# Optimization experiments

Measured on AMD Instinct MI355X. Metric: run time of the kernel, lower is better.

Reference implementation:

```python
import jax, jax.numpy as jnp
import numpy as np

N_FFT = 1024
HOP = 256
CACHE = N_FFT - 1  # causal left padding
EPS = 1e-12
BATCH = 16
SAMPLES = HOP * 2048


def _make_weight():
    # DFT basis modulated by a periodic Hann window (torch.hann_window default).
    n = np.arange(N_FFT, dtype=np.float32)
    k = np.arange(N_FFT // 2 + 1, dtype=np.float32)[:, None]
    ang = (-2.0 * np.pi / N_FFT) * k * n[None, :]
    win = 0.5 * (1.0 - np.cos(2.0 * np.pi * n / N_FFT))
    w = np.concatenate([np.cos(ang), np.sin(ang)], axis=0) * win  # [2*(N//2+1), N_FFT]
    return jnp.asarray(w, dtype=jnp.float32)[:, None, :]  # [O, I=1, K]


def setup_inputs() -> dict:
    key = jax.random.key(0)
    x = jax.random.normal(key, (BATCH, SAMPLES), dtype=jnp.float32)
    return {"x": x, "weight": _make_weight()}


def reference(x, weight):
    if x.ndim == 2:
        x = x[:, None, :]  # [B, 1, T]
    # causal constant (zero) padding on the left
    x = jnp.pad(x, ((0, 0), (0, 0), (CACHE, 0)))
    # strided conv against the fixed DFT basis: [B, 2*(N//2+1), L]
    y = jax.lax.conv_general_dilated(
        x, weight, window_strides=(HOP,), padding='VALID',
        dimension_numbers=('NCH', 'OIH', 'NCH'))
    B, C, T = y.shape
    y = y.reshape(B, 2, C // 2, T)  # real/imag split
    mag = jnp.sqrt(jnp.clip(jnp.sum(y * y, axis=1), EPS, None))  # [B, N//2+1, L]
    return mag
```

## Files before the change

kernel.cpp:

```cpp
#include <hip/hip_runtime.h>
#include <stdint.h>

#define SAMPLES   524288
#define BATCH     16
#define T_FRAMES  2048
#define HOPSZ     256
#define NCH       513
#define KF        512
#define MF        1152

#define SB_OFF    1183744
#define DB_OFF_1P (SB_OFF + 33554432)
#define WS_1P     (DB_OFF_1P + 33554432)
#define DB_OFF_2P 17960960

typedef __bf16          bf16x8 __attribute__((ext_vector_type(8)));
typedef float           f32x4  __attribute__((ext_vector_type(4)));
typedef unsigned short  u16x8  __attribute__((ext_vector_type(8)));

__device__ __forceinline__ unsigned short f2bf(float f) {
    union { float f; unsigned u; } v; v.f = f;
    unsigned r = v.u + 0x7fffu + ((v.u >> 16) & 1u);
    return (unsigned short)(r >> 16);
}

__global__ void prep(const float* __restrict__ x, const float* __restrict__ wsrc,
                     unsigned short* __restrict__ Wf,
                     unsigned short* __restrict__ Sb,
                     unsigned short* __restrict__ Db,
                     int batch0, int wblocks) {
    int bid = blockIdx.x;
    const int tid = threadIdx.x;
    if (bid < wblocks) {
        int gid = bid * 256 + tid;
        int m   = gid >> 6;
        int n0  = (gid & 63) << 3;
        int g = m >> 5, h = (m >> 4) & 1, r = m & 15;
        int bin = g * 16 + r;
        bool valid = h ? (bin >= 1 && bin <= 511) : (bin <= 512);
        const float* ws = wsrc + (long long)(h ? NCH + bin : bin) * 1024;
        union { u16x8 v; unsigned short e[8]; } o;
        #pragma unroll
        for (int e = 0; e < 8; ++e) {
            int n = n0 + e;
            float v = 0.f;
            if (valid) v = (n < 511) ? ws[n + 1] : 0.5f * ws[512];
            o.e[e] = f2bf(v);
        }
        *(u16x8*)(Wf + (long long)m * KF + n0) = o.v;
        return;
    }
    bid -= wblocks;
    const int fr = tid >> 6;
    const int n0 = (tid & 63) << 3;
    const long long f = (long long)bid * 4 + fr;
    const int bat = batch0 + (int)(f >> 11);
    const int t   = (int)(f & 2047);
    const float* xb = x + (long long)bat * SAMPLES;
    float fwd[8], rev[8];
    if (t >= 4) {
        const f32x4* pf = (const f32x4*)(xb + (t * 256 + n0 - 1024));
        f32x4 A = pf[0], B = pf[1], C = pf[2];
        fwd[0]=A[2]; fwd[1]=A[3]; fwd[2]=B[0]; fwd[3]=B[1];
        fwd[4]=B[2]; fwd[5]=B[3]; fwd[6]=C[0]; fwd[7]=C[1];
        const f32x4* pr = (const f32x4*)(xb + (t * 256 - n0 - 8));
        f32x4 D = pr[0], E = pr[1], F = pr[2];
        rev[0]=F[0]; rev[1]=E[3]; rev[2]=E[2]; rev[3]=E[1];
        rev[4]=E[0]; rev[5]=D[3]; rev[6]=D[2]; rev[7]=D[1];
    } else {
        #pragma unroll
        for (int e = 0; e < 8; ++e) {
            int n  = n0 + e;
            int pf = t * 256 + n + 1 - 1023;
            int pr = t * 256 - n;
            fwd[e] = (pf >= 0) ? xb[pf] : 0.f;
            rev[e] = (pr >= 0) ? xb[pr] : 0.f;
        }
    }
    union { u16x8 v; unsigned short e[8]; } so, dof;
    #pragma unroll
    for (int e = 0; e < 8; ++e) {
        so.e[e]  = f2bf(fwd[e] + rev[e]);
        dof.e[e] = f2bf(fwd[e] - rev[e]);
    }
    *(u16x8*)(Sb + f * KF + n0) = so.v;
    *(u16x8*)(Db + f * KF + n0) = dof.v;
}

__device__ __forceinline__ void gll16(const unsigned short* g, unsigned short* s) {
    __builtin_amdgcn_global_load_lds(
        (const __attribute__((address_space(1))) void*)g,
        (__attribute__((address_space(3))) void*)s,
        16, 0, 0);
}

__global__ __launch_bounds__(256, 3)
void stft_gemm(const unsigned short* __restrict__ Sb,
               const unsigned short* __restrict__ Db,
               const unsigned short* __restrict__ Wf,
               float* __restrict__ out, int batch0, int ftpx) {
    __shared__ unsigned short Ws[128 * 64];
    __shared__ unsigned short Ss[128 * 64];
    __shared__ unsigned short Ds[128 * 64];

    const int id  = blockIdx.x;
    const int xcd = id & 7;
    const int u   = id >> 3;
    const int ftl = u / 9;
    const int nt  = u - ftl * 9;
    const int ft  = xcd * ftpx + ftl;
    const int t0  = (ft & 15) * 128;
    const long long fl0 = (long long)ft * 128;

    const int tid = threadIdx.x;
    const int l   = tid & 63;
    const int w   = tid >> 6;
    const int ln  = l & 15;
    const int qd  = l >> 4;

    const int srow   = l >> 3;
    const int schunk = l & 7;

    const unsigned short* asrc[4];
    const unsigned short* ssrc[4];
    const unsigned short* dsrc[4];
    unsigned short* adst[4];
    unsigned short* sdst[4];
    unsigned short* ddst[4];
    #pragma unroll
    for (int c = 0; c < 4; ++c) {
        int r = w * 32 + c * 8 + srow;
        int gchunk = schunk ^ (r & 7);
        asrc[c] = Wf + (long long)(nt * 128 + r) * KF + gchunk * 8;
        ssrc[c] = Sb + (fl0 + r) * KF + gchunk * 8;
        dsrc[c] = Db + (fl0 + r) * KF + gchunk * 8;
        adst[c] = Ws + (w * 32 + c * 8) * 64;
        sdst[c] = Ss + (w * 32 + c * 8) * 64;
        ddst[c] = Ds + (w * 32 + c * 8) * 64;
    }

    const int wave_m = w & 1;
    const int wave_n = w >> 1;

    f32x4 acc[4][4];
    #pragma unroll
    for (int i = 0; i < 4; ++i)
        #pragma unroll
        for (int j = 0; j < 4; ++j)
            acc[i][j] = (f32x4){0.f, 0.f, 0.f, 0.f};

    int a_off[4][2], b_off[4][2];
    #pragma unroll
    for (int i = 0; i < 4; ++i)
        #pragma unroll
        for (int k2 = 0; k2 < 2; ++k2) {
            int ck = ((k2 * 4 + qd) ^ (ln & 7)) * 8;
            a_off[i][k2] = (wave_m * 64 + i * 16 + ln) * 64 + ck;
            b_off[i][k2] = (wave_n * 64 + i * 16 + ln) * 64 + ck;
        }

    for (int kk = 0; kk < KF; kk += 64) {
        #pragma unroll
        for (int c = 0; c < 4; ++c) gll16(asrc[c] + kk, adst[c]);
        #pragma unroll
        for (int c = 0; c < 4; ++c) gll16(ssrc[c] + kk, sdst[c]);
        #pragma unroll
        for (int c = 0; c < 4; ++c) gll16(dsrc[c] + kk, ddst[c]);
        __syncthreads();

        #pragma unroll
        for (int k2 = 0; k2 < 2; ++k2) {
            bf16x8 av[4], bs[4], bd[4];
            #pragma unroll
            for (int i = 0; i < 4; ++i) av[i] = *(const bf16x8*)&Ws[a_off[i][k2]];
            #pragma unroll
            for (int j = 0; j < 4; ++j) bs[j] = *(const bf16x8*)&Ss[b_off[j][k2]];
            #pragma unroll
            for (int j = 0; j < 4; ++j) bd[j] = *(const bf16x8*)&Ds[b_off[j][k2]];
            #pragma unroll
            for (int j = 0; j < 4; ++j) {
                acc[0][j] = __builtin_amdgcn_mfma_f32_16x16x32_bf16(av[0], bs[j], acc[0][j], 0, 0, 0);
                acc[1][j] = __builtin_amdgcn_mfma_f32_16x16x32_bf16(av[1], bd[j], acc[1][j], 0, 0, 0);
                acc[2][j] = __builtin_amdgcn_mfma_f32_16x16x32_bf16(av[2], bs[j], acc[2][j], 0, 0, 0);
                acc[3][j] = __builtin_amdgcn_mfma_f32_16x16x32_bf16(av[3], bd[j], acc[3][j], 0, 0, 0);
            }
        }
        __syncthreads();
    }

    const int b = batch0 + (ft >> 4);
    float* outb = out + (long long)b * (NCH * T_FRAMES);
    #pragma unroll
    for (int p = 0; p < 2; ++p) {
        #pragma unroll
        for (int j = 0; j < 4; ++j) {
            const int t = t0 + wave_n * 64 + j * 16 + ln;
            #pragma unroll
            for (int r = 0; r < 4; ++r) {
                float re  = acc[2 * p][j][r];
                float im  = acc[2 * p + 1][j][r];
                int bin = (nt * 4 + wave_m * 2 + p) * 16 + qd * 4 + r;
                if (bin < NCH)
                    outb[(long long)bin * T_FRAMES + t] =
                        sqrtf(fmaxf(re * re + im * im, 1e-12f));
            }
        }
    }
}

extern "C" void kernel_launch(void* const* d_in, const int* in_sizes, int n_in,
                              void* d_out, int out_size, void* d_ws, size_t ws_size,
                              hipStream_t stream) {
    const float* x  = (const float*)d_in[0];
    const float* wt = (const float*)d_in[1];
    float* out = (float*)d_out;

    unsigned short* Wf = (unsigned short*)d_ws;
    unsigned short* Sb = (unsigned short*)((char*)d_ws + SB_OFF);

    if (ws_size >= (size_t)WS_1P) {
        unsigned short* Db = (unsigned short*)((char*)d_ws + DB_OFF_1P);
        prep<<<288 + 8192, 256, 0, stream>>>(x, wt, Wf, Sb, Db, 0, 288);
        stft_gemm<<<2304, 256, 0, stream>>>(Sb, Db, Wf, out, 0, 32);
    } else {
        unsigned short* Db = (unsigned short*)((char*)d_ws + DB_OFF_2P);
        prep<<<288 + 4096, 256, 0, stream>>>(x, wt, Wf, Sb, Db, 0, 288);
        stft_gemm<<<1152, 256, 0, stream>>>(Sb, Db, Wf, out, 0, 16);
        prep<<<4096, 256, 0, stream>>>(x, wt, Wf, Sb, Db, 8, 0);
        stft_gemm<<<1152, 256, 0, stream>>>(Sb, Db, Wf, out, 8, 16);
    }
}
```

Baseline: 151.3 us.

## Compute Nyquist bin in prep and widen GEMM tile to 256 bins with 512 threads

The Nyquist bin (512) is now computed in the prep kernel as a wave-reduced dot product against the raw input sums, and it is written straight to the output. This lets the GEMM cover exactly 512 bins, i.e. 4 M-tiles of 256 instead of 9 tiles of 128 with padding waste. The GEMM block doubles to 512 threads and 8 waves, sharing each S/D tile across 256 bins. That halves the B-tile reloads and removes the padded bin rows. In exchange, prep does extra per-thread weight loads, and each block uses more LDS and larger launch bounds, which may cut occupancy.

New measurement: 143.2 us. -5.4%, faster.

```diff
diff --git a/kernel.cpp b/kernel.cpp
--- a/kernel.cpp
+++ b/kernel.cpp
@@ -7,7 +7,6 @@
 #define HOPSZ     256
 #define NCH       513
 #define KF        512
-#define MF        1152
 
 #define SB_OFF    1183744
 #define DB_OFF_1P (SB_OFF + 33554432)
@@ -28,6 +27,7 @@
                      unsigned short* __restrict__ Wf,
                      unsigned short* __restrict__ Sb,
                      unsigned short* __restrict__ Db,
+                     float* __restrict__ out,
                      int batch0, int wblocks) {
     int bid = blockIdx.x;
     const int tid = threadIdx.x;
@@ -36,15 +36,14 @@
         int m   = gid >> 6;
         int n0  = (gid & 63) << 3;
         int g = m >> 5, h = (m >> 4) & 1, r = m & 15;
-        int bin = g * 16 + r;
-        bool valid = h ? (bin >= 1 && bin <= 511) : (bin <= 512);
+        int bin  = g * 16 + r;
+        bool zero = (h == 1 && bin == 0);
         const float* ws = wsrc + (long long)(h ? NCH + bin : bin) * 1024;
         union { u16x8 v; unsigned short e[8]; } o;
         #pragma unroll
         for (int e = 0; e < 8; ++e) {
             int n = n0 + e;
-            float v = 0.f;
-            if (valid) v = (n < 511) ? ws[n + 1] : 0.5f * ws[512];
+            float v = zero ? 0.f : ((n < 511) ? ws[n + 1] : 0.5f * ws[512]);
             o.e[e] = f2bf(v);
         }
         *(u16x8*)(Wf + (long long)m * KF + n0) = o.v;
@@ -52,7 +51,8 @@
     }
     bid -= wblocks;
     const int fr = tid >> 6;
-    const int n0 = (tid & 63) << 3;
+    const int lane = tid & 63;
+    const int n0 = lane << 3;
     const long long f = (long long)bid * 4 + fr;
     const int bat = batch0 + (int)(f >> 11);
     const int t   = (int)(f & 2047);
@@ -77,14 +77,26 @@
             rev[e] = (pr >= 0) ? xb[pr] : 0.f;
         }
     }
+    const float* w512 = wsrc + (long long)512 * 1024;
+    float p512 = 0.f;
     union { u16x8 v; unsigned short e[8]; } so, dof;
     #pragma unroll
     for (int e = 0; e < 8; ++e) {
-        so.e[e]  = f2bf(fwd[e] + rev[e]);
-        dof.e[e] = f2bf(fwd[e] - rev[e]);
+        float s = fwd[e] + rev[e];
+        float d = fwd[e] - rev[e];
+        so.e[e]  = f2bf(s);
+        dof.e[e] = f2bf(d);
+        int n = n0 + e;
+        float wv = (n < 511) ? w512[n + 1] : 0.5f * w512[512];
+        p512 += wv * s;
     }
     *(u16x8*)(Sb + f * KF + n0) = so.v;
     *(u16x8*)(Db + f * KF + n0) = dof.v;
+    #pragma unroll
+    for (int off = 32; off > 0; off >>= 1) p512 += __shfl_xor(p512, off, 64);
+    if (lane == 0)
+        out[((long long)bat * NCH + 512) * T_FRAMES + t] =
+            sqrtf(fmaxf(p512 * p512, 1e-12f));
 }
 
 __device__ __forceinline__ void gll16(const unsigned short* g, unsigned short* s) {
@@ -94,20 +106,20 @@
         16, 0, 0);
 }
 
-__global__ __launch_bounds__(256, 3)
+__global__ __launch_bounds__(512, 4)
 void stft_gemm(const unsigned short* __restrict__ Sb,
                const unsigned short* __restrict__ Db,
                const unsigned short* __restrict__ Wf,
                float* __restrict__ out, int batch0, int ftpx) {
-    __shared__ unsigned short Ws[128 * 64];
+    __shared__ unsigned short As[256 * 64];
     __shared__ unsigned short Ss[128 * 64];
     __shared__ unsigned short Ds[128 * 64];
 
     const int id  = blockIdx.x;
     const int xcd = id & 7;
     const int u   = id >> 3;
-    const int ftl = u / 9;
-    const int nt  = u - ftl * 9;
+    const int ftl = u >> 2;
+    const int nt  = u & 3;
     const int ft  = xcd * ftpx + ftl;
     const int t0  = (ft & 15) * 128;
     const long long fl0 = (long long)ft * 128;
@@ -122,25 +134,25 @@
     const int schunk = l & 7;
 
     const unsigned short* asrc[4];
-    const unsigned short* ssrc[4];
-    const unsigned short* dsrc[4];
+    const unsigned short* bsrc[4];
     unsigned short* adst[4];
-    unsigned short* sdst[4];
-    unsigned short* ddst[4];
+    unsigned short* bdst[4];
+    const int wb = w & 3;
+    const unsigned short* Bglob = (w < 4) ? Sb : Db;
+    unsigned short* Blds = (w < 4) ? Ss : Ds;
     #pragma unroll
     for (int c = 0; c < 4; ++c) {
-        int r = w * 32 + c * 8 + srow;
-        int gchunk = schunk ^ (r & 7);
-        asrc[c] = Wf + (long long)(nt * 128 + r) * KF + gchunk * 8;
-        ssrc[c] = Sb + (fl0 + r) * KF + gchunk * 8;
-        dsrc[c] = Db + (fl0 + r) * KF + gchunk * 8;
-        adst[c] = Ws + (w * 32 + c * 8) * 64;
-        sdst[c] = Ss + (w * 32 + c * 8) * 64;
-        ddst[c] = Ds + (w * 32 + c * 8) * 64;
-    }
-
-    const int wave_m = w & 1;
-    const int wave_n = w >> 1;
+        int ra = w * 32 + c * 8 + srow;
+        int rb = wb * 32 + c * 8 + srow;
+        int gchunk = schunk ^ (srow & 7);
+        asrc[c] = Wf + (long long)(nt * 256 + ra) * KF + gchunk * 8;
+        bsrc[c] = Bglob + (fl0 + rb) * KF + gchunk * 8;
+        adst[c] = As + (w * 32 + c * 8) * 64;
+        bdst[c] = Blds + (wb * 32 + c * 8) * 64;
+    }
+
+    const int wave_m = w & 3;
+    const int wave_n = w >> 2;
 
     f32x4 acc[4][4];
     #pragma unroll
@@ -163,16 +175,14 @@
         #pragma unroll
         for (int c = 0; c < 4; ++c) gll16(asrc[c] + kk, adst[c]);
         #pragma unroll
-        for (int c = 0; c < 4; ++c) gll16(ssrc[c] + kk, sdst[c]);
-        #pragma unroll
-        for (int c = 0; c < 4; ++c) gll16(dsrc[c] + kk, ddst[c]);
+        for (int c = 0; c < 4; ++c) gll16(bsrc[c] + kk, bdst[c]);
         __syncthreads();
 
         #pragma unroll
         for (int k2 = 0; k2 < 2; ++k2) {
             bf16x8 av[4], bs[4], bd[4];
             #pragma unroll
-            for (int i = 0; i < 4; ++i) av[i] = *(const bf16x8*)&Ws[a_off[i][k2]];
+            for (int i = 0; i < 4; ++i) av[i] = *(const bf16x8*)&As[a_off[i][k2]];
             #pragma unroll
             for (int j = 0; j < 4; ++j) bs[j] = *(const bf16x8*)&Ss[b_off[j][k2]];
             #pragma unroll
@@ -199,10 +209,9 @@
             for (int r = 0; r < 4; ++r) {
                 float re  = acc[2 * p][j][r];
                 float im  = acc[2 * p + 1][j][r];
-                int bin = (nt * 4 + wave_m * 2 + p) * 16 + qd * 4 + r;
-                if (bin < NCH)
-                    outb[(long long)bin * T_FRAMES + t] =
-                        sqrtf(fmaxf(re * re + im * im, 1e-12f));
+                int bin = (nt * 8 + wave_m * 2 + p) * 16 + qd * 4 + r;
+                outb[(long long)bin * T_FRAMES + t] =
+                    sqrtf(fmaxf(re * re + im * im, 1e-12f));
             }
         }
     }
@@ -220,13 +229,13 @@
 
     if (ws_size >= (size_t)WS_1P) {
         unsigned short* Db = (unsigned short*)((char*)d_ws + DB_OFF_1P);
-        prep<<<288 + 8192, 256, 0, stream>>>(x, wt, Wf, Sb, Db, 0, 288);
-        stft_gemm<<<2304, 256, 0, stream>>>(Sb, Db, Wf, out, 0, 32);
+        prep<<<256 + 8192, 256, 0, stream>>>(x, wt, Wf, Sb, Db, out, 0, 256);
+        stft_gemm<<<1024, 512, 0, stream>>>(Sb, Db, Wf, out, 0, 32);
     } else {
         unsigned short* Db = (unsigned short*)((char*)d_ws + DB_OFF_2P);
-        prep<<<288 + 4096, 256, 0, stream>>>(x, wt, Wf, Sb, Db, 0, 288);
-        stft_gemm<<<1152, 256, 0, stream>>>(Sb, Db, Wf, out, 0, 16);
-        prep<<<4096, 256, 0, stream>>>(x, wt, Wf, Sb, Db, 8, 0);
-        stft_gemm<<<1152, 256, 0, stream>>>(Sb, Db, Wf, out, 8, 16);
-    }
-}
+        prep<<<256 + 4096, 256, 0, stream>>>(x, wt, Wf, Sb, Db, out, 0, 256);
+        stft_gemm<<<512, 512, 0, stream>>>(Sb, Db, Wf, out, 0, 16);
+        prep<<<4096, 256, 0, stream>>>(x, wt, Wf, Sb, Db, out, 8, 0);
+        stft_gemm<<<512, 512, 0, stream>>>(Sb, Db, Wf, out, 8, 16);
+    }
+}
```
